# Kernel tuning notes

Hardware: AMD Instinct MI355X
Metric: run time of the kernel (lower is better)

## Reference

```python
import jax, jax.numpy as jnp
import numpy as np


def setup_inputs() -> dict:
    key = jax.random.key(0)
    M, N = 2048, 16384
    x = jax.random.normal(key, (M, N), dtype=jnp.float32)
    # expk per DREAMPlace get_expk: exp(-j*pi*n/(2N)) stored as [N, 2] = (cos, -sin)
    ang = jnp.arange(N, dtype=jnp.float32) * np.float32(np.pi / (2.0 * N))
    expk = jnp.stack([jnp.cos(ang), -jnp.sin(ang)], axis=-1)
    return {"x": x, "expk": expk}


def reference(x, expk):
    """IDXCT: y_k = Re{ sum_{n=0}^{N-1} x_n * exp(j*pi/(2N) * n * (2k+1)) }.

    O(N log N) via the FFT trick:
      y_k = Re{ sum_n [x_n * exp(j*pi*n/(2N))] * exp(j*2*pi*n*k/(2N)) }
          = 2N * Re{ IFFT_{2N}(zero-padded v)[k] },  v_n = x_n * conj(expk_n)
    """
    N = x.shape[-1]
    # expk encodes exp(-j*pi*n/(2N)); we need its conjugate exp(+j*pi*n/(2N))
    v = x * (expk[..., 0] - 1j * expk[..., 1])  # complex64, [M, N]
    V = jnp.fft.ifft(v, n=2 * N, axis=-1)       # zero-padded to 2N
    y = (2 * N) * jnp.real(V[..., :N])
    return y.astype(x.dtype)
```

## Files before the change

### kernel.cpp

```cpp
#include <hip/hip_runtime.h>

#define PI_F 3.14159265358979323846f

constexpr int N_COLS   = 16384;
constexpr int HALF     = 8192;
constexpr int NTHREADS = 1024;

__global__ __launch_bounds__(NTHREADS)
void idxct_kernel(const float* __restrict__ x,
                  const float* __restrict__ expk,
                  float* __restrict__ y)
{
    __shared__ float sre[HALF];
    __shared__ float sim[HALF];

    const int row = blockIdx.x;
    const float* __restrict__ xr = x + (size_t)row * N_COLS;
    float* __restrict__ yr       = y + (size_t)row * N_COLS;
    const int t = threadIdx.x;
    const float x0 = xr[0];
    const float2* __restrict__ ek2 = (const float2*)expk;

    #pragma unroll
    for (int i = 0; i < HALF / NTHREADS; ++i) {
        int k = t + i * NTHREADS;
        float vkr, vki;
        {
            float2 e = ek2[k];
            float c = e.x, s = -e.y;
            if (k == 0) { vkr = x0; vki = 0.0f; }
            else {
                float a = xr[k], b = xr[N_COLS - k];
                vkr = a * c + b * s;
                vki = a * s - b * c;
            }
        }
        float wkr, wki;
        {
            int K = k + HALF;
            float2 e = ek2[K];
            float c = e.x, s = -e.y;
            float a = xr[K], b = xr[N_COLS - K];
            wkr = a * c + b * s;
            wki = a * s - b * c;
        }
        float dr = vkr - wkr, di = vki - wki;
        float ang = (2.0f * PI_F / (float)N_COLS) * (float)k;
        float es, ec;
        __sincosf(ang, &es, &ec);
        float zr = (vkr + wkr) - (ec * di + es * dr);
        float zi = (vki + wki) + (ec * dr - es * di);
        int rk = (int)(__brev((unsigned)k) >> 19);
        sre[rk] = zr;
        sim[rk] = zi;
    }

    #pragma unroll
    for (int p = 0; p < 6; ++p) {
        const int s  = 1 << (2 * p);
        __syncthreads();
        #pragma unroll
        for (int u = 0; u < 2; ++u) {
            int q   = t + u * NTHREADS;
            int j   = q & (s - 1);
            int base = ((q >> (2 * p)) << (2 * p + 2)) + j;
            float r0 = sre[base],           i0 = sim[base];
            float r1 = sre[base + s],       i1 = sim[base + s];
            float r2 = sre[base + 2 * s],   i2 = sim[base + 2 * s];
            float r3 = sre[base + 3 * s],   i3 = sim[base + 3 * s];
            float a1 = (float)j * (PI_F / (float)s);
            float s1, c1; __sincosf(a1, &s1, &c1);
            float a2 = (float)j * (PI_F / (float)(2 * s));
            float s2, c2; __sincosf(a2, &s2, &c2);
            float tr, ti;
            tr = c1 * r1 - s1 * i1; ti = c1 * i1 + s1 * r1;
            r1 = r0 - tr; i1 = i0 - ti; r0 += tr; i0 += ti;
            tr = c1 * r3 - s1 * i3; ti = c1 * i3 + s1 * r3;
            r3 = r2 - tr; i3 = i2 - ti; r2 += tr; i2 += ti;
            tr = c2 * r2 - s2 * i2; ti = c2 * i2 + s2 * r2;
            r2 = r0 - tr; i2 = i0 - ti; r0 += tr; i0 += ti;
            tr = -s2 * r3 - c2 * i3; ti = c2 * r3 - s2 * i3;
            r3 = r1 - tr; i3 = i1 - ti; r1 += tr; i1 += ti;
            sre[base]         = r0; sim[base]         = i0;
            sre[base + s]     = r1; sim[base + s]     = i1;
            sre[base + 2 * s] = r2; sim[base + 2 * s] = i2;
            sre[base + 3 * s] = r3; sim[base + 3 * s] = i3;
        }
    }

    __syncthreads();
    #pragma unroll
    for (int u = 0; u < 4; ++u) {
        int q = t + u * NTHREADS;
        float a = (float)q * (PI_F / 4096.0f);
        float sn, cs; __sincosf(a, &sn, &cs);
        float r0 = sre[q],        i0 = sim[q];
        float r1 = sre[q + 4096], i1 = sim[q + 4096];
        float tr = cs * r1 - sn * i1;
        float ti = cs * i1 + sn * r1;
        sre[q]        = r0 + tr; sim[q]        = i0 + ti;
        sre[q + 4096] = r0 - tr; sim[q + 4096] = i0 - ti;
    }
    __syncthreads();

    #pragma unroll
    for (int i = 0; i < N_COLS / NTHREADS; ++i) {
        int q = t + i * NTHREADS;
        int pidx = (q & 1) ? (N_COLS - 1 - (q >> 1)) : (q >> 1);
        int zi = pidx >> 1;
        float val = (pidx & 1) ? sim[zi] : sre[zi];
        yr[q] = 0.5f * (val + x0);
    }
}

extern "C" void kernel_launch(void* const* d_in, const int* in_sizes, int n_in,
                              void* d_out, int out_size, void* d_ws, size_t ws_size,
                              hipStream_t stream)
{
    const float* x    = (const float*)d_in[0];
    const float* expk = (const float*)d_in[1];
    float* y          = (float*)d_out;
    const int M = in_sizes[0] / N_COLS;
    idxct_kernel<<<dim3(M), dim3(NTHREADS), 0, stream>>>(x, expk, y);
}
```

Before: 280.1 us.

## Swizzle shared-memory FFT layout and derive twiddles algebraically

Applies an XOR swizzle to every shared-memory index across all FFT stages to break LDS bank conflicts from power-of-two strides. The first radix-4 stage is special-cased with trivial twiddles, so its sincos and multiplies are dropped. Other twiddles come from double-angle identities instead of extra __sincosf calls, and the pre-twiddle reuses expk squared twice. This trades transcendental work for a few FMAs, with small accuracy drift from the repeated squaring.

Result: faster. 257.2 us (-8.2%).

```diff
diff --git a/kernel.cpp b/kernel.cpp
--- a/kernel.cpp
+++ b/kernel.cpp
@@ -5,6 +5,10 @@
 constexpr int N_COLS   = 16384;
 constexpr int HALF     = 8192;
 constexpr int NTHREADS = 1024;
+
+__device__ __forceinline__ int sw(int a) {
+    return a ^ ((a >> 5) & 31) ^ ((a >> 10) & 31);
+}
 
 __global__ __launch_bounds__(NTHREADS)
 void idxct_kernel(const float* __restrict__ x,
@@ -24,15 +28,15 @@
     #pragma unroll
     for (int i = 0; i < HALF / NTHREADS; ++i) {
         int k = t + i * NTHREADS;
-        float vkr, vki;
+        float vkr, vki, c0, s0;
         {
             float2 e = ek2[k];
-            float c = e.x, s = -e.y;
+            c0 = e.x; s0 = -e.y;
             if (k == 0) { vkr = x0; vki = 0.0f; }
             else {
                 float a = xr[k], b = xr[N_COLS - k];
-                vkr = a * c + b * s;
-                vki = a * s - b * c;
+                vkr = a * c0 + b * s0;
+                vki = a * s0 - b * c0;
             }
         }
         float wkr, wki;
@@ -45,33 +49,58 @@
             wki = a * s - b * c;
         }
         float dr = vkr - wkr, di = vki - wki;
-        float ang = (2.0f * PI_F / (float)N_COLS) * (float)k;
-        float es, ec;
-        __sincosf(ang, &es, &ec);
+        float cA = c0 * c0 - s0 * s0, sA = 2.0f * c0 * s0;
+        float ec = cA * cA - sA * sA, es = 2.0f * cA * sA;
         float zr = (vkr + wkr) - (ec * di + es * dr);
         float zi = (vki + wki) + (ec * dr - es * di);
         int rk = (int)(__brev((unsigned)k) >> 19);
-        sre[rk] = zr;
-        sim[rk] = zi;
+        int pa = sw(rk);
+        sre[pa] = zr;
+        sim[pa] = zi;
+    }
+
+    __syncthreads();
+    #pragma unroll
+    for (int u = 0; u < 2; ++u) {
+        int q = t + u * NTHREADS;
+        int a0 = sw(q << 2);
+        int a1 = a0 ^ 1, a2i = a0 ^ 2, a3 = a0 ^ 3;
+        float r0 = sre[a0],  i0 = sim[a0];
+        float r1 = sre[a1],  i1 = sim[a1];
+        float r2 = sre[a2i], i2 = sim[a2i];
+        float r3 = sre[a3],  i3 = sim[a3];
+        float tr, ti;
+        tr = r1;  ti = i1;  r1 = r0 - tr; i1 = i0 - ti; r0 += tr; i0 += ti;
+        tr = r3;  ti = i3;  r3 = r2 - tr; i3 = i2 - ti; r2 += tr; i2 += ti;
+        tr = r2;  ti = i2;  r2 = r0 - tr; i2 = i0 - ti; r0 += tr; i0 += ti;
+        tr = -i3; ti = r3;  r3 = r1 - tr; i3 = i1 - ti; r1 += tr; i1 += ti;
+        sre[a0]  = r0; sim[a0]  = i0;
+        sre[a1]  = r1; sim[a1]  = i1;
+        sre[a2i] = r2; sim[a2i] = i2;
+        sre[a3]  = r3; sim[a3]  = i3;
     }
 
     #pragma unroll
-    for (int p = 0; p < 6; ++p) {
-        const int s  = 1 << (2 * p);
+    for (int p = 1; p < 6; ++p) {
+        const int s = 1 << (2 * p);
         __syncthreads();
         #pragma unroll
         for (int u = 0; u < 2; ++u) {
-            int q   = t + u * NTHREADS;
-            int j   = q & (s - 1);
+            int q = t + u * NTHREADS;
+            int j = q & (s - 1);
             int base = ((q >> (2 * p)) << (2 * p + 2)) + j;
-            float r0 = sre[base],           i0 = sim[base];
-            float r1 = sre[base + s],       i1 = sim[base + s];
-            float r2 = sre[base + 2 * s],   i2 = sim[base + 2 * s];
-            float r3 = sre[base + 3 * s],   i3 = sim[base + 3 * s];
-            float a1 = (float)j * (PI_F / (float)s);
-            float s1, c1; __sincosf(a1, &s1, &c1);
-            float a2 = (float)j * (PI_F / (float)(2 * s));
-            float s2, c2; __sincosf(a2, &s2, &c2);
+            int a0 = sw(base);
+            int a1 = sw(base + s);
+            int a2i = sw(base + 2 * s);
+            int a3 = sw(base + 3 * s);
+            float r0 = sre[a0],  i0 = sim[a0];
+            float r1 = sre[a1],  i1 = sim[a1];
+            float r2 = sre[a2i], i2 = sim[a2i];
+            float r3 = sre[a3],  i3 = sim[a3];
+            float a2ang = (float)j * (PI_F / (float)(2 * s));
+            float s2, c2; __sincosf(a2ang, &s2, &c2);
+            float c1 = c2 * c2 - s2 * s2;
+            float s1 = 2.0f * c2 * s2;
             float tr, ti;
             tr = c1 * r1 - s1 * i1; ti = c1 * i1 + s1 * r1;
             r1 = r0 - tr; i1 = i0 - ti; r0 += tr; i0 += ti;
@@ -81,10 +110,10 @@
             r2 = r0 - tr; i2 = i0 - ti; r0 += tr; i0 += ti;
             tr = -s2 * r3 - c2 * i3; ti = c2 * r3 - s2 * i3;
             r3 = r1 - tr; i3 = i1 - ti; r1 += tr; i1 += ti;
-            sre[base]         = r0; sim[base]         = i0;
-            sre[base + s]     = r1; sim[base + s]     = i1;
-            sre[base + 2 * s] = r2; sim[base + 2 * s] = i2;
-            sre[base + 3 * s] = r3; sim[base + 3 * s] = i3;
+            sre[a0]  = r0; sim[a0]  = i0;
+            sre[a1]  = r1; sim[a1]  = i1;
+            sre[a2i] = r2; sim[a2i] = i2;
+            sre[a3]  = r3; sim[a3]  = i3;
         }
     }
 
@@ -94,12 +123,14 @@
         int q = t + u * NTHREADS;
         float a = (float)q * (PI_F / 4096.0f);
         float sn, cs; __sincosf(a, &sn, &cs);
-        float r0 = sre[q],        i0 = sim[q];
-        float r1 = sre[q + 4096], i1 = sim[q + 4096];
+        int a0 = sw(q);
+        int a1 = sw(q + 4096);
+        float r0 = sre[a0], i0 = sim[a0];
+        float r1 = sre[a1], i1 = sim[a1];
         float tr = cs * r1 - sn * i1;
         float ti = cs * i1 + sn * r1;
-        sre[q]        = r0 + tr; sim[q]        = i0 + ti;
-        sre[q + 4096] = r0 - tr; sim[q + 4096] = i0 - ti;
+        sre[a0] = r0 + tr; sim[a0] = i0 + ti;
+        sre[a1] = r0 - tr; sim[a1] = i0 - ti;
     }
     __syncthreads();
 
@@ -107,7 +138,7 @@
     for (int i = 0; i < N_COLS / NTHREADS; ++i) {
         int q = t + i * NTHREADS;
         int pidx = (q & 1) ? (N_COLS - 1 - (q >> 1)) : (q >> 1);
-        int zi = pidx >> 1;
+        int zi = sw(pidx >> 1);
         float val = (pidx & 1) ? sim[zi] : sre[zi];
         yr[q] = 0.5f * (val + x0);
     }
```

## Restructure in-block FFT as radix-8 passes with register first stage and swizzled LDS

Applied to the files above, without the earlier changes.

Replaces the radix-4 shared-memory FFT (six radix-4 passes plus a radix-2 pass, with a bit-reversal scatter) with a decimation-in-frequency radix-8 scheme. The first radix-8 stage runs in registers right after the pre-twiddle, then three LDS passes follow, and the final radix-2 is folded into the output gather. Twiddles come from angle-doubling of expk and a recurrence in place of many sincos calls. An XOR swizzle on LDS addresses is meant to avoid bank conflicts. This cuts LDS round-trips and barriers, but adds index arithmetic and may lose some accuracy from the recurrence-based twiddles.

Result: faster. 265.4 us (-5.3%).

```diff
diff --git a/kernel.cpp b/kernel.cpp
--- a/kernel.cpp
+++ b/kernel.cpp
@@ -2,114 +2,150 @@
 
 #define PI_F 3.14159265358979323846f
 
-constexpr int N_COLS   = 16384;
-constexpr int HALF     = 8192;
-constexpr int NTHREADS = 1024;
+constexpr int N_COLS = 16384;
+constexpr int HALF   = 8192;
+constexpr int NT     = 1024;
 
-__global__ __launch_bounds__(NTHREADS)
+__device__ __forceinline__ int swz(int a) {
+    return a ^ ((a >> 3) & 31) ^ ((a >> 8) & 31);
+}
+
+__device__ __forceinline__ void bfly8_tw(float (&vr)[8], float (&vi)[8],
+                                         float ct, float st)
+{
+    const float RS = 0.70710678118654752f;
+    float e0r = vr[0]+vr[4], e0i = vi[0]+vi[4];
+    float e1r = vr[0]-vr[4], e1i = vi[0]-vi[4];
+    float e2r = vr[2]+vr[6], e2i = vi[2]+vi[6];
+    float e3r = vr[2]-vr[6], e3i = vi[2]-vi[6];
+    float A0r = e0r+e2r, A0i = e0i+e2i;
+    float A2r = e0r-e2r, A2i = e0i-e2i;
+    float A1r = e1r-e3i, A1i = e1i+e3r;
+    float A3r = e1r+e3i, A3i = e1i-e3r;
+    float o0r = vr[1]+vr[5], o0i = vi[1]+vi[5];
+    float o1r = vr[1]-vr[5], o1i = vi[1]-vi[5];
+    float o2r = vr[3]+vr[7], o2i = vi[3]+vi[7];
+    float o3r = vr[3]-vr[7], o3i = vi[3]-vi[7];
+    float B0r = o0r+o2r, B0i = o0i+o2i;
+    float B2r = o0r-o2r, B2i = o0i-o2i;
+    float B1r = o1r-o3i, B1i = o1i+o3r;
+    float B3r = o1r+o3i, B3i = o1i-o3r;
+    float t;
+    t = RS*(B1r - B1i); B1i = RS*(B1r + B1i); B1r = t;
+    t = -B2i;           B2i = B2r;            B2r = t;
+    t = -RS*(B3r + B3i); B3i = RS*(B3r - B3i); B3r = t;
+    vr[0]=A0r+B0r; vi[0]=A0i+B0i;  vr[4]=A0r-B0r; vi[4]=A0i-B0i;
+    vr[1]=A1r+B1r; vi[1]=A1i+B1i;  vr[5]=A1r-B1r; vi[5]=A1i-B1i;
+    vr[2]=A2r+B2r; vi[2]=A2i+B2i;  vr[6]=A2r-B2r; vi[6]=A2i-B2i;
+    vr[3]=A3r+B3r; vi[3]=A3i+B3i;  vr[7]=A3r-B3r; vi[7]=A3i-B3i;
+    float wr = ct, wi = st;
+    #pragma unroll
+    for (int i = 1; i < 8; ++i) {
+        float xr2 = vr[i]*wr - vi[i]*wi;
+        float xi2 = vr[i]*wi + vi[i]*wr;
+        vr[i] = xr2; vi[i] = xi2;
+        if (i < 7) { float nr = wr*ct - wi*st, ni = wr*st + wi*ct; wr = nr; wi = ni; }
+    }
+}
+
+template<int S>
+__device__ __forceinline__ void lds_pass(float* sdata, int b)
+{
+    const int j = b & (S - 1);
+    const int base = ((b & ~(S - 1)) << 3) + j;
+    int pa[8];
+    float vr[8], vi[8];
+    #pragma unroll
+    for (int r = 0; r < 8; ++r) {
+        pa[r] = swz(base + S * r);
+        vr[r] = sdata[pa[r]];
+        vi[r] = sdata[HALF + pa[r]];
+    }
+    float st, ct;
+    __sincosf((float)j * (PI_F / (4.0f * (float)S)), &st, &ct);
+    bfly8_tw(vr, vi, ct, st);
+    #pragma unroll
+    for (int i = 0; i < 8; ++i) {
+        sdata[pa[i]]        = vr[i];
+        sdata[HALF + pa[i]] = vi[i];
+    }
+}
+
+__global__ __launch_bounds__(NT, 8)
 void idxct_kernel(const float* __restrict__ x,
                   const float* __restrict__ expk,
                   float* __restrict__ y)
 {
-    __shared__ float sre[HALF];
-    __shared__ float sim[HALF];
+    __shared__ float sdata[2 * HALF];
 
     const int row = blockIdx.x;
     const float* __restrict__ xr = x + (size_t)row * N_COLS;
-    float* __restrict__ yr       = y + (size_t)row * N_COLS;
-    const int t = threadIdx.x;
+    float* __restrict__ yrp      = y + (size_t)row * N_COLS;
+    const int b = threadIdx.x;
     const float x0 = xr[0];
     const float2* __restrict__ ek2 = (const float2*)expk;
 
+    float vr[8], vi[8];
+
     #pragma unroll
-    for (int i = 0; i < HALF / NTHREADS; ++i) {
-        int k = t + i * NTHREADS;
-        float vkr, vki;
-        {
-            float2 e = ek2[k];
-            float c = e.x, s = -e.y;
-            if (k == 0) { vkr = x0; vki = 0.0f; }
-            else {
-                float a = xr[k], b = xr[N_COLS - k];
-                vkr = a * c + b * s;
-                vki = a * s - b * c;
-            }
-        }
-        float wkr, wki;
-        {
-            int K = k + HALF;
-            float2 e = ek2[K];
-            float c = e.x, s = -e.y;
-            float a = xr[K], b = xr[N_COLS - K];
-            wkr = a * c + b * s;
-            wki = a * s - b * c;
-        }
+    for (int r = 0; r < 8; ++r) {
+        int k = b + (r << 10);
+        float2 e = ek2[k];
+        float c0 = e.x, s0 = -e.y;
+        int kb = (k == 0) ? 0 : (N_COLS - k);
+        float a  = xr[k], bb = xr[kb];
+        float vkr = a * c0 + bb * s0;
+        float vki = a * s0 - bb * c0;
+        if (k == 0) { vkr = x0; vki = 0.0f; }
+        int K = k + HALF;
+        float2 e2 = ek2[K];
+        float c1 = e2.x, s1 = -e2.y;
+        float aa = xr[K], b2 = xr[N_COLS - K];
+        float wkr = aa * c1 + b2 * s1;
+        float wki = aa * s1 - b2 * c1;
         float dr = vkr - wkr, di = vki - wki;
-        float ang = (2.0f * PI_F / (float)N_COLS) * (float)k;
-        float es, ec;
-        __sincosf(ang, &es, &ec);
-        float zr = (vkr + wkr) - (ec * di + es * dr);
-        float zi = (vki + wki) + (ec * dr - es * di);
-        int rk = (int)(__brev((unsigned)k) >> 19);
-        sre[rk] = zr;
-        sim[rk] = zi;
+        float cA = c0 * c0 - s0 * s0, sA = 2.0f * c0 * s0;
+        float ec = cA * cA - sA * sA, es = 2.0f * cA * sA;
+        vr[r] = (vkr + wkr) - (ec * di + es * dr);
+        vi[r] = (vki + wki) + (ec * dr - es * di);
     }
 
-    #pragma unroll
-    for (int p = 0; p < 6; ++p) {
-        const int s  = 1 << (2 * p);
-        __syncthreads();
+    {
+        float st, ct;
+        __sincosf((float)b * (PI_F / 4096.0f), &st, &ct);
+        bfly8_tw(vr, vi, ct, st);
         #pragma unroll
-        for (int u = 0; u < 2; ++u) {
-            int q   = t + u * NTHREADS;
-            int j   = q & (s - 1);
-            int base = ((q >> (2 * p)) << (2 * p + 2)) + j;
-            float r0 = sre[base],           i0 = sim[base];
-            float r1 = sre[base + s],       i1 = sim[base + s];
-            float r2 = sre[base + 2 * s],   i2 = sim[base + 2 * s];
-            float r3 = sre[base + 3 * s],   i3 = sim[base + 3 * s];
-            float a1 = (float)j * (PI_F / (float)s);
-            float s1, c1; __sincosf(a1, &s1, &c1);
-            float a2 = (float)j * (PI_F / (float)(2 * s));
-            float s2, c2; __sincosf(a2, &s2, &c2);
-            float tr, ti;
-            tr = c1 * r1 - s1 * i1; ti = c1 * i1 + s1 * r1;
-            r1 = r0 - tr; i1 = i0 - ti; r0 += tr; i0 += ti;
-            tr = c1 * r3 - s1 * i3; ti = c1 * i3 + s1 * r3;
-            r3 = r2 - tr; i3 = i2 - ti; r2 += tr; i2 += ti;
-            tr = c2 * r2 - s2 * i2; ti = c2 * i2 + s2 * r2;
-            r2 = r0 - tr; i2 = i0 - ti; r0 += tr; i0 += ti;
-            tr = -s2 * r3 - c2 * i3; ti = c2 * r3 - s2 * i3;
-            r3 = r1 - tr; i3 = i1 - ti; r1 += tr; i1 += ti;
-            sre[base]         = r0; sim[base]         = i0;
-            sre[base + s]     = r1; sim[base + s]     = i1;
-            sre[base + 2 * s] = r2; sim[base + 2 * s] = i2;
-            sre[base + 3 * s] = r3; sim[base + 3 * s] = i3;
+        for (int i = 0; i < 8; ++i) {
+            int pa = swz(b + (i << 10));
+            sdata[pa]        = vr[i];
+            sdata[HALF + pa] = vi[i];
         }
     }
 
     __syncthreads();
-    #pragma unroll
-    for (int u = 0; u < 4; ++u) {
-        int q = t + u * NTHREADS;
-        float a = (float)q * (PI_F / 4096.0f);
-        float sn, cs; __sincosf(a, &sn, &cs);
-        float r0 = sre[q],        i0 = sim[q];
-        float r1 = sre[q + 4096], i1 = sim[q + 4096];
-        float tr = cs * r1 - sn * i1;
-        float ti = cs * i1 + sn * r1;
-        sre[q]        = r0 + tr; sim[q]        = i0 + ti;
-        sre[q + 4096] = r0 - tr; sim[q + 4096] = i0 - ti;
-    }
+    lds_pass<128>(sdata, b);
+    __syncthreads();
+    lds_pass<16>(sdata, b);
+    __syncthreads();
+    lds_pass<2>(sdata, b);
     __syncthreads();
 
     #pragma unroll
-    for (int i = 0; i < N_COLS / NTHREADS; ++i) {
-        int q = t + i * NTHREADS;
-        int pidx = (q & 1) ? (N_COLS - 1 - (q >> 1)) : (q >> 1);
-        int zi = pidx >> 1;
-        float val = (pidx & 1) ? sim[zi] : sre[zi];
-        yr[q] = 0.5f * (val + x0);
+    for (int i = 0; i < 16; ++i) {
+        int q = b + (i << 10);
+        int qh = q >> 1;
+        int pidx = (q & 1) ? (N_COLS - 1 - qh) : qh;
+        int comp = (pidx & 1) << 13;
+        int m = pidx >> 1;
+        int j5 = m >> 12;
+        int mm = m & 4095;
+        int pe = ((mm & 7) << 10) | (((mm >> 3) & 7) << 7)
+               | (((mm >> 6) & 7) << 4) | (((mm >> 9) & 7) << 1);
+        int a0 = swz(pe);
+        float v0 = sdata[comp + a0];
+        float v1 = sdata[comp + (a0 ^ 1)];
+        float val = j5 ? (v0 - v1) : (v0 + v1);
+        yrp[q] = 0.5f * (val + x0);
     }
 }
 
@@ -121,5 +157,5 @@
     const float* expk = (const float*)d_in[1];
     float* y          = (float*)d_out;
     const int M = in_sizes[0] / N_COLS;
-    idxct_kernel<<<dim3(M), dim3(NTHREADS), 0, stream>>>(x, expk, y);
+    idxct_kernel<<<dim3(M), dim3(NT), 0, stream>>>(x, expk, y);
 }
```
